# Performance work log

Measured on AMD Instinct MI355X. Metric: run time of the kernel, lower is better.

The kernel has to match this reference:

```python
import jax, jax.numpy as jnp
import numpy as np

CAPACITY_FACTOR = 1.25
TOP_K = 2


def setup_inputs() -> dict:
    key = jax.random.key(0)
    ks = jax.random.split(key, 4)
    B, T, D, H, N = 8, 8192, 512, 512, 32
    x = jax.random.normal(ks[0], (B, T, D), jnp.float32)
    Wg = jax.random.normal(ks[1], (D, N), jnp.float32) * 0.02   # gate (no bias)
    W1 = jax.random.normal(ks[2], (N, D, H), jnp.float32) * 0.02  # stacked expert fc1
    b1 = jnp.zeros((N, H), jnp.float32)
    W2 = jax.random.normal(ks[3], (N, H, D), jnp.float32) * 0.02  # stacked expert fc2
    b2 = jnp.zeros((N, D), jnp.float32)
    return {"x": x, "Wg": Wg, "W1": W1, "b1": b1, "W2": W2, "b2": b2}


def _moe(x, Wg, W1, b1, W2, b2):
    B, T, D = x.shape
    N = Wg.shape[1]
    K = TOP_K
    BT = B * T
    BTK = BT * K
    C = int(np.ceil(CAPACITY_FACTOR * BTK / N))  # capacity per expert (static)

    x_flat = x.reshape(BT, D)
    probs = jax.nn.softmax(x_flat @ Wg, axis=-1)            # [BT, N]
    vals, idx = jax.lax.top_k(probs, K)                     # [BT, K]
    vals = vals / jnp.clip(vals.sum(-1, keepdims=True), 1e-9)  # normalize_gates

    # Assignments in the exact order of the original double loop: pos-major, j-minor.
    a = idx.reshape(BTK)                                    # expert id per assignment
    oh = jax.nn.one_hot(a, N, dtype=jnp.int32)              # [BTK, N]
    rank = jnp.cumsum(oh, axis=0) - oh                      # prior count for each expert
    pos = jnp.take_along_axis(rank, a[:, None], axis=1)[:, 0]  # slot within expert
    keep = pos < C                                          # capacity-limited dispatch
    dest = jnp.where(keep, a * C + pos, N * C)              # OOB sentinel -> dropped
    token = jnp.arange(BTK) // K                            # source token per assignment

    # Dispatch: scatter kept tokens into per-expert capacity buffers [N, C, D].
    buf = jnp.zeros((N * C, D), x.dtype).at[dest].set(x_flat[token], mode="drop")
    buf = buf.reshape(N, C, D)

    # Expert FFN (grouped GEMMs). FeedForwardExpert assumed Linear-ReLU-Linear.
    h = jax.nn.relu(jnp.einsum("ncd,ndh->nch", buf, W1) + b1[:, None, :])
    o = (jnp.einsum("nch,nhd->ncd", h, W2) + b2[:, None, :]).reshape(N * C, D)

    # Combine: gather expert outputs, weight by gates, scatter-add back by token.
    gathered = o[jnp.minimum(dest, N * C - 1)]              # dropped rows zeroed via w
    w = vals.reshape(BTK) * keep.astype(x.dtype)
    y_flat = jax.ops.segment_sum(gathered * w[:, None], token, num_segments=BT)
    contrib = jax.ops.segment_sum(w, token, num_segments=BT)
    # Tokens with no surviving assignment pass through unchanged.
    y_flat = jnp.where(contrib[:, None] <= 1e-12, x_flat, y_flat)
    return y_flat.reshape(B, T, D)


def reference(x, Wg, W1, b1, W2, b2):
    return _moe(x, Wg, W1, b1, W2, b2)
```

## Files before the change

kernel.cpp:

```cpp
#include <hip/hip_runtime.h>
#include <hip/hip_bf16.h>

#define BT 65536
#define DD 512
#define HH 512
#define NE 32
#define CAP 5120
#define BM 64
#define NRB 80

typedef float  f32x4  __attribute__((ext_vector_type(4)));
typedef short  bf16x8 __attribute__((ext_vector_type(8)));

__device__ __forceinline__ unsigned short f2bf(float f){
    unsigned int u = __builtin_bit_cast(unsigned int, f);
    unsigned int r = (u + 0x7fffu + ((u >> 16) & 1u)) >> 16;
    return (unsigned short)r;
}
__device__ __forceinline__ float bf2f(unsigned short h){
    unsigned int u = ((unsigned int)h) << 16;
    return __builtin_bit_cast(float, u);
}

__global__ __launch_bounds__(256) void k_prep(
    const float* __restrict__ x, const float* __restrict__ Wg,
    const float* __restrict__ W1, const float* __restrict__ W2,
    unsigned short* __restrict__ W1f, unsigned short* __restrict__ W2f,
    int* __restrict__ counts, int* __restrict__ gsl, float* __restrict__ wts,
    unsigned char* __restrict__ flags, unsigned short* __restrict__ xb16)
{
    __shared__ float WgS[DD * NE];
    __shared__ int lcnt[NE], lbase[NE];

    int tid = threadIdx.x;

    if (blockIdx.x >= 256){
        int b = blockIdx.x - 256;
        int w = b >> 8;
        int e = (b >> 3) & 31;
        int kq = b & 7;
        const float* src = (w ? W2 : W1) + ((size_t)e << 18);
        unsigned short* dst = (w ? W2f : W1f) + ((size_t)e << 18);
        int n4 = (tid & 127) * 4;
        int kh = tid >> 7;
        #pragma unroll 1
        for (int kg = 0; kg < 4; kg++){
            int k0 = kq*64 + (kg*2 + kh)*8;
            float4 rows[8];
            #pragma unroll
            for (int j = 0; j < 8; j++)
                rows[j] = *(const float4*)&src[(size_t)(k0 + j)*512 + n4];
            unsigned short v0[8], v1[8], v2[8], v3[8];
            #pragma unroll
            for (int j = 0; j < 8; j++){
                v0[j] = f2bf(rows[j].x); v1[j] = f2bf(rows[j].y);
                v2[j] = f2bf(rows[j].z); v3[j] = f2bf(rows[j].w);
            }
            int kc = k0 >> 5, lb = ((k0 >> 3) & 3)*16;
            #pragma unroll
            for (int m = 0; m < 4; m++){
                int n = n4 + m;
                int nt = n >> 4, ln = lb + (n & 15);
                const unsigned short* vv = (m==0)?v0:(m==1)?v1:(m==2)?v2:v3;
                *(bf16x8*)(dst + (((size_t)(nt*16 + kc)*64 + ln) << 3)) = *(const bf16x8*)vv;
            }
        }
        return;
    }

    int tok = blockIdx.x * 256 + tid;
    const float* xr = x + (size_t)tok * DD;

    #pragma unroll
    for (int i = 0; i < 16; i++){
        int f = i*1024 + tid*4;
        *(float4*)&WgS[f] = *(const float4*)&Wg[f];
    }
    if (tid < NE) lcnt[tid] = 0;
    __syncthreads();

    float acc[NE];
    #pragma unroll
    for (int n = 0; n < NE; n++) acc[n] = 0.f;

    float4 xa = *(const float4*)(xr);
    float4 xb = *(const float4*)(xr + 4);
    #pragma unroll 1
    for (int d = 0; d < DD; d += 8){
        int dn = (d + 8 < DD) ? (d + 8) : 0;
        float4 na = *(const float4*)(xr + dn);
        float4 nb = *(const float4*)(xr + dn + 4);
        uint4 pk;
        pk.x = (unsigned)f2bf(xa.x) | ((unsigned)f2bf(xa.y) << 16);
        pk.y = (unsigned)f2bf(xa.z) | ((unsigned)f2bf(xa.w) << 16);
        pk.z = (unsigned)f2bf(xb.x) | ((unsigned)f2bf(xb.y) << 16);
        pk.w = (unsigned)f2bf(xb.z) | ((unsigned)f2bf(xb.w) << 16);
        *(uint4*)(xb16 + (size_t)tok*DD + d) = pk;
        #pragma unroll
        for (int j = 0; j < 8; j++){
            float xv = (j < 4) ? ((j==0)?xa.x:(j==1)?xa.y:(j==2)?xa.z:xa.w)
                               : ((j==4)?xb.x:(j==5)?xb.y:(j==6)?xb.z:xb.w);
            const float4* wr = (const float4*)&WgS[(d + j)*NE];
            #pragma unroll
            for (int q = 0; q < 8; q++){
                float4 w4 = wr[q];
                acc[q*4+0] = fmaf(xv, w4.x, acc[q*4+0]);
                acc[q*4+1] = fmaf(xv, w4.y, acc[q*4+1]);
                acc[q*4+2] = fmaf(xv, w4.z, acc[q*4+2]);
                acc[q*4+3] = fmaf(xv, w4.w, acc[q*4+3]);
            }
        }
        xa = na; xb = nb;
    }

    float v1 = -1e30f; int i1 = -1;
    #pragma unroll
    for (int n = 0; n < NE; n++) if (acc[n] > v1){ v1 = acc[n]; i1 = n; }
    float v2 = -1e30f; int i2 = -1;
    #pragma unroll
    for (int n = 0; n < NE; n++) if (n != i1 && acc[n] > v2){ v2 = acc[n]; i2 = n; }
    float v3 = -1e30f;
    #pragma unroll
    for (int n = 0; n < NE; n++) if (n != i1 && n != i2 && acc[n] > v3) v3 = acc[n];

    float w1, w2;
    if (v2 - v3 >= 1e-4f){
        double ex  = exp((double)v2 - (double)v1);
        double inv = 1.0 / (1.0 + ex);
        w1 = (float)inv; w2 = (float)(ex * inv);
    } else {
        float thresh = v2 - 1e-3f;
        unsigned cmask = 0u;
        #pragma unroll
        for (int n = 0; n < NE; n++) cmask |= (acc[n] >= thresh) ? (1u << n) : 0u;

        double dv1 = -1.0e300, dv2 = -1.0e300; int di1 = -1, di2 = -1;
        #pragma unroll 1
        for (int n = 0; n < NE; n++){
            if (!((cmask >> n) & 1u)) continue;
            double s0 = 0.0, s1 = 0.0, s2 = 0.0, s3 = 0.0;
            #pragma unroll 4
            for (int d = 0; d < DD; d += 4){
                s0 = fma((double)xr[d+0], (double)Wg[(size_t)(d+0)*NE + n], s0);
                s1 = fma((double)xr[d+1], (double)Wg[(size_t)(d+1)*NE + n], s1);
                s2 = fma((double)xr[d+2], (double)Wg[(size_t)(d+2)*NE + n], s2);
                s3 = fma((double)xr[d+3], (double)Wg[(size_t)(d+3)*NE + n], s3);
            }
            double s = (s0 + s1) + (s2 + s3);
            if (s > dv1){ dv2 = dv1; di2 = di1; dv1 = s; di1 = n; }
            else if (s > dv2){ dv2 = s; di2 = n; }
        }
        i1 = di1; i2 = di2;
        double ex  = exp(dv2 - dv1);
        double inv = 1.0 / (1.0 + ex);
        w1 = (float)inv; w2 = (float)(ex * inv);
    }

    int s1 = atomicAdd(&lcnt[i1], 1);
    int s2 = atomicAdd(&lcnt[i2], 1);
    __syncthreads();
    if (tid < NE && lcnt[tid] > 0) lbase[tid] = atomicAdd(&counts[tid], lcnt[tid]);
    __syncthreads();
    int g1 = lbase[i1] + s1;
    int g2 = lbase[i2] + s2;
    bool k1 = g1 < CAP, k2 = g2 < CAP;
    if (k1){ gsl[i1*CAP + g1] = tok;               wts[i1*CAP + g1] = w1; }
    if (k2){ gsl[i2*CAP + g2] = tok | (1 << 20);   wts[i2*CAP + g2] = w2; }
    flags[tok] = (unsigned char)((k1 ? 1 : 0) | (k2 ? 2 : 0));
}

__global__ __launch_bounds__(512, 4) void k_ffn(
    const unsigned short* __restrict__ xb16,
    const unsigned short* __restrict__ W1f,
    const unsigned short* __restrict__ W2f,
    const float* __restrict__ b1, const float* __restrict__ b2,
    const int* __restrict__ counts,
    const int* __restrict__ gsl, const float* __restrict__ wts,
    float* __restrict__ y, unsigned short* __restrict__ y2h)
{
    __shared__ unsigned char AH[64 * 1024];

    int p  = blockIdx.x;
    int s  = p >> 3;
    int e  = ((s / NRB) << 3) | (p & 7);
    int rb = s % NRB;

    int cnt = counts[e]; if (cnt > CAP) cnt = CAP;
    int r0 = rb * BM;
    if (r0 >= cnt) return;

    int tid  = threadIdx.x;
    int lane = tid & 63;
    int wv   = tid >> 6;
    int lg   = lane >> 4;
    int ll   = lane & 15;

    {
        int row = tid >> 3, seg = tid & 7;
        int gr  = r0 + row;
        char* rowb = (char*)AH + row * 1024;
        int rsw = (row & 7) << 4;
        if (gr < cnt){
            int tk = gsl[e*CAP + gr] & 0xFFFFF;
            const uint4* src = (const uint4*)(xb16 + (size_t)tk*DD + seg*64);
            #pragma unroll
            for (int j = 0; j < 8; j++){
                uint4 v = src[j];
                int chunk = seg*8 + j;
                *(uint4*)(rowb + ((chunk << 4) ^ rsw)) = v;
            }
        } else {
            uint4 zz; zz.x = zz.y = zz.z = zz.w = 0u;
            #pragma unroll
            for (int j = 0; j < 8; j++){
                int chunk = seg*8 + j;
                *(uint4*)(rowb + ((chunk << 4) ^ rsw)) = zz;
            }
        }
    }
    __syncthreads();

    f32x4 acc[4][4];
    #pragma unroll
    for (int a2 = 0; a2 < 4; a2++)
        #pragma unroll
        for (int tt = 0; tt < 4; tt++)
            acc[a2][tt] = (f32x4)0.f;

    {
        const unsigned short* Wa = W1f + ((size_t)e << 18) + (size_t)wv*32768;
        bf16x8 f0[4], f1[4];
        #pragma unroll
        for (int a2 = 0; a2 < 4; a2++)
            f0[a2] = *(const bf16x8*)(Wa + a2*8192 + lane*8);
        #pragma unroll 1
        for (int c = 0; c < 16; c += 2){
            #pragma unroll
            for (int a2 = 0; a2 < 4; a2++)
                f1[a2] = *(const bf16x8*)(Wa + a2*8192 + (c+1)*512 + lane*8);
            {
                bf16x8 bx[4];
                #pragma unroll
                for (int tt = 0; tt < 4; tt++){
                    int tok = tt*16 + ll;
                    int bofs = (64*c + 16*lg) ^ ((tok & 7) << 4);
                    bx[tt] = *(const bf16x8*)((char*)AH + tok*1024 + bofs);
                }
                __builtin_amdgcn_s_setprio(1);
                #pragma unroll
                for (int a2 = 0; a2 < 4; a2++)
                    #pragma unroll
                    for (int tt = 0; tt < 4; tt++)
                        acc[a2][tt] = __builtin_amdgcn_mfma_f32_16x16x32_bf16(f0[a2], bx[tt], acc[a2][tt], 0, 0, 0);
                __builtin_amdgcn_s_setprio(0);
            }
            if (c + 2 < 16){
                #pragma unroll
                for (int a2 = 0; a2 < 4; a2++)
                    f0[a2] = *(const bf16x8*)(Wa + a2*8192 + (c+2)*512 + lane*8);
            }
            {
                bf16x8 bx[4];
                #pragma unroll
                for (int tt = 0; tt < 4; tt++){
                    int tok = tt*16 + ll;
                    int bofs = (64*(c+1) + 16*lg) ^ ((tok & 7) << 4);
                    bx[tt] = *(const bf16x8*)((char*)AH + tok*1024 + bofs);
                }
                __builtin_amdgcn_s_setprio(1);
                #pragma unroll
                for (int a2 = 0; a2 < 4; a2++)
                    #pragma unroll
                    for (int tt = 0; tt < 4; tt++)
                        acc[a2][tt] = __builtin_amdgcn_mfma_f32_16x16x32_bf16(f1[a2], bx[tt], acc[a2][tt], 0, 0, 0);
                __builtin_amdgcn_s_setprio(0);
            }
        }
    }
    __syncthreads();

    #pragma unroll
    for (int a2 = 0; a2 < 4; a2++){
        int n0 = wv*64 + a2*16 + lg*4;
        float4 bv = *(const float4*)(b1 + e*HH + n0);
        #pragma unroll
        for (int tt = 0; tt < 4; tt++){
            int tok = tt*16 + ll;
            float h0 = acc[a2][tt][0] + bv.x; h0 = h0 > 0.f ? h0 : 0.f;
            float h1 = acc[a2][tt][1] + bv.y; h1 = h1 > 0.f ? h1 : 0.f;
            float h2 = acc[a2][tt][2] + bv.z; h2 = h2 > 0.f ? h2 : 0.f;
            float h3 = acc[a2][tt][3] + bv.w; h3 = h3 > 0.f ? h3 : 0.f;
            uint2 pk;
            pk.x = (unsigned)f2bf(h0) | ((unsigned)f2bf(h1) << 16);
            pk.y = (unsigned)f2bf(h2) | ((unsigned)f2bf(h3) << 16);
            int bofs = (n0*2) ^ ((tok & 7) << 4);
            *(uint2*)((char*)AH + tok*1024 + bofs) = pk;
            acc[a2][tt] = (f32x4)0.f;
        }
    }
    __syncthreads();

    {
        const unsigned short* Wb = W2f + ((size_t)e << 18) + (size_t)wv*32768;
        bf16x8 f0[4], f1[4];
        #pragma unroll
        for (int b_ = 0; b_ < 4; b_++)
            f0[b_] = *(const bf16x8*)(Wb + b_*8192 + lane*8);
        #pragma unroll 1
        for (int kc = 0; kc < 16; kc += 2){
            #pragma unroll
            for (int b_ = 0; b_ < 4; b_++)
                f1[b_] = *(const bf16x8*)(Wb + b_*8192 + (kc+1)*512 + lane*8);
            {
                bf16x8 ah[4];
                #pragma unroll
                for (int tt = 0; tt < 4; tt++){
                    int tok = tt*16 + ll;
                    int bofs = (64*kc + 16*lg) ^ ((tok & 7) << 4);
                    ah[tt] = *(const bf16x8*)((char*)AH + tok*1024 + bofs);
                }
                __builtin_amdgcn_s_setprio(1);
                #pragma unroll
                for (int b_ = 0; b_ < 4; b_++)
                    #pragma unroll
                    for (int tt = 0; tt < 4; tt++)
                        acc[b_][tt] = __builtin_amdgcn_mfma_f32_16x16x32_bf16(ah[tt], f0[b_], acc[b_][tt], 0, 0, 0);
                __builtin_amdgcn_s_setprio(0);
            }
            if (kc + 2 < 16){
                #pragma unroll
                for (int b_ = 0; b_ < 4; b_++)
                    f0[b_] = *(const bf16x8*)(Wb + b_*8192 + (kc+2)*512 + lane*8);
            }
            {
                bf16x8 ah[4];
                #pragma unroll
                for (int tt = 0; tt < 4; tt++){
                    int tok = tt*16 + ll;
                    int bofs = (64*(kc+1) + 16*lg) ^ ((tok & 7) << 4);
                    ah[tt] = *(const bf16x8*)((char*)AH + tok*1024 + bofs);
                }
                __builtin_amdgcn_s_setprio(1);
                #pragma unroll
                for (int b_ = 0; b_ < 4; b_++)
                    #pragma unroll
                    for (int tt = 0; tt < 4; tt++)
                        acc[b_][tt] = __builtin_amdgcn_mfma_f32_16x16x32_bf16(ah[tt], f1[b_], acc[b_][tt], 0, 0, 0);
                __builtin_amdgcn_s_setprio(0);
            }
        }
    }

    float bb[4];
    #pragma unroll
    for (int b_ = 0; b_ < 4; b_++)
        bb[b_] = b2[e*DD + wv*64 + b_*16 + ll];

    #pragma unroll
    for (int tt = 0; tt < 4; tt++){
        #pragma unroll
        for (int i = 0; i < 4; i++){
            int rl = tt*16 + lg*4 + i;
            int gr = r0 + rl;
            if (gr < cnt){
                int   v  = gsl[e*CAP + gr];
                int   tk = v & 0xFFFFF;
                float w  = wts[e*CAP + gr];
                if (v >> 20){
                    unsigned short* dst = y2h + (size_t)tk * DD;
                    #pragma unroll
                    for (int b_ = 0; b_ < 4; b_++){
                        int col = wv*64 + b_*16 + ll;
                        dst[col] = f2bf(w * (acc[b_][tt][i] + bb[b_]));
                    }
                } else {
                    float* dst = y + (size_t)tk * DD;
                    #pragma unroll
                    for (int b_ = 0; b_ < 4; b_++){
                        int col = wv*64 + b_*16 + ll;
                        dst[col] = w * (acc[b_][tt][i] + bb[b_]);
                    }
                }
            }
        }
    }
}

__global__ __launch_bounds__(256) void k_comb(
    const float* __restrict__ x, const unsigned short* __restrict__ y2h,
    const unsigned char* __restrict__ flags, float* __restrict__ y)
{
    const float4* x4  = (const float4*)x;
    const uint2*  y24 = (const uint2*)y2h;
    float4* y4 = (float4*)y;
    int nthreads = gridDim.x * 256;
    int g = blockIdx.x * 256 + threadIdx.x;
    #pragma unroll 1
    for (long long idx = g; idx < (long long)BT * 128; idx += nthreads){
        int t = (int)(idx >> 7);
        int f = flags[t];
        if (f == 3){
            float4 a = y4[idx];
            uint2 p = y24[idx];
            a.x += bf2f((unsigned short)(p.x & 0xFFFF));
            a.y += bf2f((unsigned short)(p.x >> 16));
            a.z += bf2f((unsigned short)(p.y & 0xFFFF));
            a.w += bf2f((unsigned short)(p.y >> 16));
            y4[idx] = a;
        } else if (f == 2){
            uint2 p = y24[idx];
            float4 a;
            a.x = bf2f((unsigned short)(p.x & 0xFFFF));
            a.y = bf2f((unsigned short)(p.x >> 16));
            a.z = bf2f((unsigned short)(p.y & 0xFFFF));
            a.w = bf2f((unsigned short)(p.y >> 16));
            y4[idx] = a;
        } else if (f == 0){
            y4[idx] = x4[idx];
        }
    }
}

extern "C" void kernel_launch(void* const* d_in, const int* in_sizes, int n_in,
                              void* d_out, int out_size, void* d_ws, size_t ws_size,
                              hipStream_t stream)
{
    const float* x  = (const float*)d_in[0];
    const float* Wg = (const float*)d_in[1];
    const float* W1 = (const float*)d_in[2];
    const float* b1 = (const float*)d_in[3];
    const float* W2 = (const float*)d_in[4];
    const float* b2 = (const float*)d_in[5];
    float* y = (float*)d_out;

    char* ws = (char*)d_ws;
    unsigned short* W1f = (unsigned short*)(ws);
    unsigned short* W2f = (unsigned short*)(ws + 16777216);
    int*   counts = (int*)  (ws + 33554432);
    int*   gsl    = (int*)  (ws + 33554432 + 256);
    float* wts    = (float*)(ws + 33554432 + 256 + 655360);
    unsigned char* flags = (unsigned char*)(ws + 33554432 + 256 + 2*655360);
    unsigned short* xb16 = (unsigned short*)(ws + 35651584);
    unsigned short* y2h  = (unsigned short*)(ws + 35651584 + 67108864);

    hipMemsetAsync(counts, 0, 256, stream);
    hipLaunchKernelGGL(k_prep, dim3(256 + 512), dim3(256), 0, stream,
                       x, Wg, W1, W2, W1f, W2f, counts, gsl, wts, flags, xb16);
    hipLaunchKernelGGL(k_ffn,  dim3(NE*NRB), dim3(512), 0, stream,
                       xb16, W1f, W2f, b1, b2, counts, gsl, wts, y, y2h);
    hipLaunchKernelGGL(k_comb, dim3(2048), dim3(256), 0, stream, x, y2h, flags, y);
}
```

Measured before the change: 405.5 us.

## Compute gating logits with split-bf16 MFMA instead of scalar FP32 FMAs

The gate projection x@Wg now runs on MFMA using a hi/lo bf16 split (three products) to approximate FP32 accuracy. A new one-block kernel pre-swizzles Wg into hi/lo fragments, and k_prep now handles 32 tokens per block staged in swizzled LDS. Top-k selection is done by 32 threads per block. The aim is to remove the scalar FMA-bound router loop, at the cost of an extra launch and the loss of the dropped lo*lo term, which could change near-tie routing.

```diff
diff --git a/kernel.cpp b/kernel.cpp
--- a/kernel.cpp
+++ b/kernel.cpp
@@ -22,20 +22,47 @@
     return __builtin_bit_cast(float, u);
 }
 
+__global__ __launch_bounds__(256) void k_wgprep(
+    const float* __restrict__ Wg,
+    unsigned short* __restrict__ WgHf, unsigned short* __restrict__ WgLf)
+{
+    int t = threadIdx.x;
+    #pragma unroll
+    for (int i = 0; i < 8; i++){
+        int entry = i*256 + t;
+        int ln = entry & 63;
+        unsigned short h[8], l[8];
+        #pragma unroll
+        for (int j = 0; j < 8; j++){
+            int d = ((entry >> 6) & 15)*32 + (ln >> 4)*8 + j;
+            int e = (entry >> 10)*16 + (ln & 15);
+            float v = Wg[d*NE + e];
+            unsigned short hi = f2bf(v);
+            h[j] = hi;
+            l[j] = f2bf(v - bf2f(hi));
+        }
+        *(bf16x8*)(WgHf + (size_t)entry*8) = *(bf16x8*)h;
+        *(bf16x8*)(WgLf + (size_t)entry*8) = *(bf16x8*)l;
+    }
+}
+
 __global__ __launch_bounds__(256) void k_prep(
     const float* __restrict__ x, const float* __restrict__ Wg,
     const float* __restrict__ W1, const float* __restrict__ W2,
+    const unsigned short* __restrict__ WgHf, const unsigned short* __restrict__ WgLf,
     unsigned short* __restrict__ W1f, unsigned short* __restrict__ W2f,
     int* __restrict__ counts, int* __restrict__ gsl, float* __restrict__ wts,
     unsigned char* __restrict__ flags, unsigned short* __restrict__ xb16)
 {
-    __shared__ float WgS[DD * NE];
+    __shared__ unsigned char XH[32 * 1024];
+    __shared__ unsigned char XL[32 * 1024];
+    __shared__ float lg2[32 * 33];
     __shared__ int lcnt[NE], lbase[NE];
 
     int tid = threadIdx.x;
 
-    if (blockIdx.x >= 256){
-        int b = blockIdx.x - 256;
+    if (blockIdx.x >= 2048){
+        int b = blockIdx.x - 2048;
         int w = b >> 8;
         int e = (b >> 3) & 31;
         int kq = b & 7;
@@ -68,105 +95,126 @@
         return;
     }
 
-    int tok = blockIdx.x * 256 + tid;
-    const float* xr = x + (size_t)tok * DD;
-
-    #pragma unroll
-    for (int i = 0; i < 16; i++){
-        int f = i*1024 + tid*4;
-        *(float4*)&WgS[f] = *(const float4*)&Wg[f];
+    int t0 = blockIdx.x * 32;
+
+    {
+        int row = tid >> 3, seg = tid & 7;
+        int tok = t0 + row;
+        const float* sx = x + (size_t)tok*DD + seg*64;
+        char* rbH = (char*)XH + row*1024;
+        char* rbL = (char*)XL + row*1024;
+        int rsw = (row & 7) << 4;
+        #pragma unroll
+        for (int jj = 0; jj < 8; jj++){
+            float4 a = *(const float4*)(sx + jj*8);
+            float4 b = *(const float4*)(sx + jj*8 + 4);
+            unsigned short h[8], l[8];
+            h[0]=f2bf(a.x); h[1]=f2bf(a.y); h[2]=f2bf(a.z); h[3]=f2bf(a.w);
+            h[4]=f2bf(b.x); h[5]=f2bf(b.y); h[6]=f2bf(b.z); h[7]=f2bf(b.w);
+            l[0]=f2bf(a.x-bf2f(h[0])); l[1]=f2bf(a.y-bf2f(h[1]));
+            l[2]=f2bf(a.z-bf2f(h[2])); l[3]=f2bf(a.w-bf2f(h[3]));
+            l[4]=f2bf(b.x-bf2f(h[4])); l[5]=f2bf(b.y-bf2f(h[5]));
+            l[6]=f2bf(b.z-bf2f(h[6])); l[7]=f2bf(b.w-bf2f(h[7]));
+            int chunk = seg*8 + jj;
+            *(bf16x8*)(rbH + ((chunk << 4) ^ rsw)) = *(bf16x8*)h;
+            *(bf16x8*)(rbL + ((chunk << 4) ^ rsw)) = *(bf16x8*)l;
+            *(bf16x8*)(xb16 + (size_t)tok*DD + seg*64 + jj*8) = *(bf16x8*)h;
+        }
     }
     if (tid < NE) lcnt[tid] = 0;
     __syncthreads();
 
-    float acc[NE];
-    #pragma unroll
-    for (int n = 0; n < NE; n++) acc[n] = 0.f;
-
-    float4 xa = *(const float4*)(xr);
-    float4 xb = *(const float4*)(xr + 4);
-    #pragma unroll 1
-    for (int d = 0; d < DD; d += 8){
-        int dn = (d + 8 < DD) ? (d + 8) : 0;
-        float4 na = *(const float4*)(xr + dn);
-        float4 nb = *(const float4*)(xr + dn + 4);
-        uint4 pk;
-        pk.x = (unsigned)f2bf(xa.x) | ((unsigned)f2bf(xa.y) << 16);
-        pk.y = (unsigned)f2bf(xa.z) | ((unsigned)f2bf(xa.w) << 16);
-        pk.z = (unsigned)f2bf(xb.x) | ((unsigned)f2bf(xb.y) << 16);
-        pk.w = (unsigned)f2bf(xb.z) | ((unsigned)f2bf(xb.w) << 16);
-        *(uint4*)(xb16 + (size_t)tok*DD + d) = pk;
-        #pragma unroll
-        for (int j = 0; j < 8; j++){
-            float xv = (j < 4) ? ((j==0)?xa.x:(j==1)?xa.y:(j==2)?xa.z:xa.w)
-                               : ((j==4)?xb.x:(j==5)?xb.y:(j==6)?xb.z:xb.w);
-            const float4* wr = (const float4*)&WgS[(d + j)*NE];
-            #pragma unroll
-            for (int q = 0; q < 8; q++){
-                float4 w4 = wr[q];
-                acc[q*4+0] = fmaf(xv, w4.x, acc[q*4+0]);
-                acc[q*4+1] = fmaf(xv, w4.y, acc[q*4+1]);
-                acc[q*4+2] = fmaf(xv, w4.z, acc[q*4+2]);
-                acc[q*4+3] = fmaf(xv, w4.w, acc[q*4+3]);
-            }
-        }
-        xa = na; xb = nb;
-    }
-
-    float v1 = -1e30f; int i1 = -1;
-    #pragma unroll
-    for (int n = 0; n < NE; n++) if (acc[n] > v1){ v1 = acc[n]; i1 = n; }
-    float v2 = -1e30f; int i2 = -1;
-    #pragma unroll
-    for (int n = 0; n < NE; n++) if (n != i1 && acc[n] > v2){ v2 = acc[n]; i2 = n; }
-    float v3 = -1e30f;
-    #pragma unroll
-    for (int n = 0; n < NE; n++) if (n != i1 && n != i2 && acc[n] > v3) v3 = acc[n];
-
-    float w1, w2;
-    if (v2 - v3 >= 1e-4f){
-        double ex  = exp((double)v2 - (double)v1);
-        double inv = 1.0 / (1.0 + ex);
-        w1 = (float)inv; w2 = (float)(ex * inv);
-    } else {
-        float thresh = v2 - 1e-3f;
-        unsigned cmask = 0u;
-        #pragma unroll
-        for (int n = 0; n < NE; n++) cmask |= (acc[n] >= thresh) ? (1u << n) : 0u;
-
-        double dv1 = -1.0e300, dv2 = -1.0e300; int di1 = -1, di2 = -1;
+    {
+        int lane = tid & 63;
+        int wv   = tid >> 6;
+        int lg   = lane >> 4, ll = lane & 15;
+        int ef = wv >> 1, tf = wv & 1;
+        const unsigned short* Ah = WgHf + ef*8192;
+        const unsigned short* Al = WgLf + ef*8192;
+        int tokl = tf*16 + ll;
+        f32x4 acc = (f32x4)0.f;
         #pragma unroll 1
-        for (int n = 0; n < NE; n++){
-            if (!((cmask >> n) & 1u)) continue;
-            double s0 = 0.0, s1 = 0.0, s2 = 0.0, s3 = 0.0;
-            #pragma unroll 4
-            for (int d = 0; d < DD; d += 4){
-                s0 = fma((double)xr[d+0], (double)Wg[(size_t)(d+0)*NE + n], s0);
-                s1 = fma((double)xr[d+1], (double)Wg[(size_t)(d+1)*NE + n], s1);
-                s2 = fma((double)xr[d+2], (double)Wg[(size_t)(d+2)*NE + n], s2);
-                s3 = fma((double)xr[d+3], (double)Wg[(size_t)(d+3)*NE + n], s3);
-            }
-            double s = (s0 + s1) + (s2 + s3);
-            if (s > dv1){ dv2 = dv1; di2 = di1; dv1 = s; di1 = n; }
-            else if (s > dv2){ dv2 = s; di2 = n; }
-        }
-        i1 = di1; i2 = di2;
-        double ex  = exp(dv2 - dv1);
-        double inv = 1.0 / (1.0 + ex);
-        w1 = (float)inv; w2 = (float)(ex * inv);
-    }
-
-    int s1 = atomicAdd(&lcnt[i1], 1);
-    int s2 = atomicAdd(&lcnt[i2], 1);
+        for (int kc = 0; kc < 16; kc++){
+            bf16x8 ah = *(const bf16x8*)(Ah + kc*512 + lane*8);
+            bf16x8 al = *(const bf16x8*)(Al + kc*512 + lane*8);
+            int bofs = (64*kc + 16*lg) ^ ((tokl & 7) << 4);
+            bf16x8 bh = *(const bf16x8*)((char*)XH + tokl*1024 + bofs);
+            bf16x8 bl = *(const bf16x8*)((char*)XL + tokl*1024 + bofs);
+            acc = __builtin_amdgcn_mfma_f32_16x16x32_bf16(ah, bh, acc, 0, 0, 0);
+            acc = __builtin_amdgcn_mfma_f32_16x16x32_bf16(ah, bl, acc, 0, 0, 0);
+            acc = __builtin_amdgcn_mfma_f32_16x16x32_bf16(al, bh, acc, 0, 0, 0);
+        }
+        #pragma unroll
+        for (int i = 0; i < 4; i++)
+            lg2[tokl*33 + ef*16 + lg*4 + i] = acc[i];
+    }
+    __syncthreads();
+
+    float w1 = 0.f, w2 = 0.f;
+    int i1 = 0, i2 = 0, s1 = 0, s2 = 0;
+    bool act = (tid < 32);
+    if (act){
+        int tok = t0 + tid;
+        float acc[NE];
+        #pragma unroll
+        for (int n = 0; n < NE; n++) acc[n] = lg2[tid*33 + n];
+
+        float v1 = -1e30f; i1 = -1;
+        #pragma unroll
+        for (int n = 0; n < NE; n++) if (acc[n] > v1){ v1 = acc[n]; i1 = n; }
+        float v2 = -1e30f; i2 = -1;
+        #pragma unroll
+        for (int n = 0; n < NE; n++) if (n != i1 && acc[n] > v2){ v2 = acc[n]; i2 = n; }
+        float v3 = -1e30f;
+        #pragma unroll
+        for (int n = 0; n < NE; n++) if (n != i1 && n != i2 && acc[n] > v3) v3 = acc[n];
+
+        if (v2 - v3 >= 1e-4f){
+            double ex  = exp((double)v2 - (double)v1);
+            double inv = 1.0 / (1.0 + ex);
+            w1 = (float)inv; w2 = (float)(ex * inv);
+        } else {
+            const float* xr = x + (size_t)tok * DD;
+            float thresh = v2 - 1e-3f;
+            unsigned cmask = 0u;
+            #pragma unroll
+            for (int n = 0; n < NE; n++) cmask |= (acc[n] >= thresh) ? (1u << n) : 0u;
+            double dv1 = -1.0e300, dv2 = -1.0e300; int di1 = -1, di2 = -1;
+            #pragma unroll 1
+            for (int n = 0; n < NE; n++){
+                if (!((cmask >> n) & 1u)) continue;
+                double q0 = 0.0, q1 = 0.0, q2 = 0.0, q3 = 0.0;
+                #pragma unroll 4
+                for (int d = 0; d < DD; d += 4){
+                    q0 = fma((double)xr[d+0], (double)Wg[(size_t)(d+0)*NE + n], q0);
+                    q1 = fma((double)xr[d+1], (double)Wg[(size_t)(d+1)*NE + n], q1);
+                    q2 = fma((double)xr[d+2], (double)Wg[(size_t)(d+2)*NE + n], q2);
+                    q3 = fma((double)xr[d+3], (double)Wg[(size_t)(d+3)*NE + n], q3);
+                }
+                double sv = (q0 + q1) + (q2 + q3);
+                if (sv > dv1){ dv2 = dv1; di2 = di1; dv1 = sv; di1 = n; }
+                else if (sv > dv2){ dv2 = sv; di2 = n; }
+            }
+            i1 = di1; i2 = di2;
+            double ex  = exp(dv2 - dv1);
+            double inv = 1.0 / (1.0 + ex);
+            w1 = (float)inv; w2 = (float)(ex * inv);
+        }
+        s1 = atomicAdd(&lcnt[i1], 1);
+        s2 = atomicAdd(&lcnt[i2], 1);
+    }
     __syncthreads();
     if (tid < NE && lcnt[tid] > 0) lbase[tid] = atomicAdd(&counts[tid], lcnt[tid]);
     __syncthreads();
-    int g1 = lbase[i1] + s1;
-    int g2 = lbase[i2] + s2;
-    bool k1 = g1 < CAP, k2 = g2 < CAP;
-    if (k1){ gsl[i1*CAP + g1] = tok;               wts[i1*CAP + g1] = w1; }
-    if (k2){ gsl[i2*CAP + g2] = tok | (1 << 20);   wts[i2*CAP + g2] = w2; }
-    flags[tok] = (unsigned char)((k1 ? 1 : 0) | (k2 ? 2 : 0));
+    if (act){
+        int tok = t0 + tid;
+        int g1 = lbase[i1] + s1;
+        int g2 = lbase[i2] + s2;
+        bool k1 = g1 < CAP, k2 = g2 < CAP;
+        if (k1){ gsl[i1*CAP + g1] = tok;               wts[i1*CAP + g1] = w1; }
+        if (k2){ gsl[i2*CAP + g2] = tok | (1 << 20);   wts[i2*CAP + g2] = w2; }
+        flags[tok] = (unsigned char)((k1 ? 1 : 0) | (k2 ? 2 : 0));
+    }
 }
 
 __global__ __launch_bounds__(512, 4) void k_ffn(
@@ -436,16 +484,20 @@
     char* ws = (char*)d_ws;
     unsigned short* W1f = (unsigned short*)(ws);
     unsigned short* W2f = (unsigned short*)(ws + 16777216);
-    int*   counts = (int*)  (ws + 33554432);
-    int*   gsl    = (int*)  (ws + 33554432 + 256);
-    float* wts    = (float*)(ws + 33554432 + 256 + 655360);
-    unsigned char* flags = (unsigned char*)(ws + 33554432 + 256 + 2*655360);
+    size_t b3 = 33554432;
+    int*   counts = (int*)  (ws + b3);
+    int*   gsl    = (int*)  (ws + b3 + 256);
+    float* wts    = (float*)(ws + b3 + 256 + 655360);
+    unsigned char* flags = (unsigned char*)(ws + b3 + 256 + 2*655360);
+    unsigned short* WgHf = (unsigned short*)(ws + b3 + 256 + 2*655360 + 65536);
+    unsigned short* WgLf = (unsigned short*)(ws + b3 + 256 + 2*655360 + 65536 + 32768);
     unsigned short* xb16 = (unsigned short*)(ws + 35651584);
     unsigned short* y2h  = (unsigned short*)(ws + 35651584 + 67108864);
 
     hipMemsetAsync(counts, 0, 256, stream);
-    hipLaunchKernelGGL(k_prep, dim3(256 + 512), dim3(256), 0, stream,
-                       x, Wg, W1, W2, W1f, W2f, counts, gsl, wts, flags, xb16);
+    hipLaunchKernelGGL(k_wgprep, dim3(1), dim3(256), 0, stream, Wg, WgHf, WgLf);
+    hipLaunchKernelGGL(k_prep, dim3(2048 + 512), dim3(256), 0, stream,
+                       x, Wg, W1, W2, WgHf, WgLf, W1f, W2f, counts, gsl, wts, flags, xb16);
     hipLaunchKernelGGL(k_ffn,  dim3(NE*NRB), dim3(512), 0, stream,
                        xb16, W1f, W2f, b1, b2, counts, gsl, wts, y, y2h);
     hipLaunchKernelGGL(k_comb, dim3(2048), dim3(256), 0, stream, x, y2h, flags, y);
```

Result: faster. 394.7 us (-2.7%).
